# Performance work log

Hardware: AMD Instinct MI355X
Metric: run time of the kernel (lower is better)

## Reference

```python
import jax, jax.numpy as jnp
import numpy as np

N_NODES = 100000
N_EDGES = 800000
N_GRAPHS = 256
IN_C = 96
HID = 96
OUT_C = 16


def setup_inputs() -> dict:
    key = jax.random.key(0)
    ks = jax.random.split(key, 10)
    x = jax.random.normal(ks[0], (N_NODES, IN_C), dtype=jnp.float32)
    edge_index = jax.random.randint(ks[1], (2, N_EDGES), 0, N_NODES, dtype=jnp.int64)
    batch = jnp.sort(jax.random.randint(ks[2], (N_NODES,), 0, N_GRAPHS, dtype=jnp.int64))
    def glorot(k, fan_in, fan_out):
        s = np.sqrt(6.0 / (fan_in + fan_out)).astype(np.float32)
        return jax.random.uniform(k, (fan_in, fan_out), minval=-s, maxval=s, dtype=jnp.float32)
    W1 = glorot(ks[3], IN_C, HID)
    W2 = glorot(ks[4], HID, HID)
    W3 = glorot(ks[5], HID, HID)
    Wlin = glorot(ks[6], HID, OUT_C)
    b1 = jnp.zeros((HID,), dtype=jnp.float32)
    b2 = jnp.zeros((HID,), dtype=jnp.float32)
    b3 = jnp.zeros((HID,), dtype=jnp.float32)
    return {"x": x, "edge_index": edge_index, "batch": batch,
            "W1": W1, "b1": b1, "W2": W2, "b2": b2, "W3": W3, "b3": b3, "Wlin": Wlin}


def _gcn_conv(x, W, b, src, dst):
    # PyG GCNConv(normalize=True): add self-loops, deg includes self-loop,
    # norm_ij = deg_i^{-1/2} * deg_j^{-1/2}; linear (no bias) then scatter-add; bias after.
    n = x.shape[0]
    deg = jnp.zeros((n,), dtype=x.dtype).at[dst].add(1.0) + 1.0  # +1 self-loop
    dinv = jax.lax.rsqrt(deg)
    h = x @ W                                   # [N, H]
    coef = dinv[src] * dinv[dst]                # [E]
    msg = h[src] * coef[:, None]                # [E, H] gather
    agg = jax.ops.segment_sum(msg, dst, num_segments=n)  # scatter-add
    agg = agg + h * (dinv * dinv)[:, None]      # self-loop contribution
    return agg + b


def reference(x, edge_index, batch, W1, b1, W2, b2, W3, b3, Wlin):
    src, dst = edge_index[0], edge_index[1]
    h = jax.nn.relu(_gcn_conv(x, W1, b1, src, dst))
    h = jax.nn.relu(_gcn_conv(h, W2, b2, src, dst))
    h = _gcn_conv(h, W3, b3, src, dst)
    # global mean pool over graphs
    sums = jax.ops.segment_sum(h, batch, num_segments=N_GRAPHS)
    counts = jax.ops.segment_sum(jnp.ones((h.shape[0],), dtype=h.dtype), batch, num_segments=N_GRAPHS)
    pooled = sums / jnp.maximum(counts, 1.0)[:, None]
    return pooled @ Wlin
```

## Files before the change

kernel.cpp:

```cpp
#include <hip/hip_runtime.h>

#define NN 100000
#define NE 800000
#define NG 256
#define CH 96
#define OC 16
#define NBLK 391
#define TM 128
#define GBLK 782

typedef __attribute__((ext_vector_type(8))) short bf16x8;
typedef __attribute__((ext_vector_type(4))) float f32x4;

__device__ __forceinline__ unsigned short f2bf(float x) {
    unsigned u = __float_as_uint(x);
    return (unsigned short)((u + 0x7fffu + ((u >> 16) & 1u)) >> 16);
}
__device__ __forceinline__ float bf2f(unsigned short h) {
    return __uint_as_float(((unsigned)h) << 16);
}
__device__ __forceinline__ void split8(const float4 a, const float4 b,
                                       bf16x8& hi, bf16x8& lo) {
    float v[8] = {a.x, a.y, a.z, a.w, b.x, b.y, b.z, b.w};
#pragma unroll
    for (int j = 0; j < 8; j++) {
        unsigned short h = f2bf(v[j]);
        hi[j] = (short)h;
        lo[j] = (short)f2bf(v[j] - bf2f(h));
    }
}
__device__ __forceinline__ void unpack8(uint4 v, float* f) {
    f[0] = __uint_as_float(v.x << 16); f[1] = __uint_as_float(v.x & 0xffff0000u);
    f[2] = __uint_as_float(v.y << 16); f[3] = __uint_as_float(v.y & 0xffff0000u);
    f[4] = __uint_as_float(v.z << 16); f[5] = __uint_as_float(v.z & 0xffff0000u);
    f[6] = __uint_as_float(v.w << 16); f[7] = __uint_as_float(v.w & 0xffff0000u);
}

__global__ __launch_bounds__(256) void k_init(int* __restrict__ cntp,
                                              int* __restrict__ gtot,
                                              const float* __restrict__ W1,
                                              const float* __restrict__ W2,
                                              const float* __restrict__ W3,
                                              const float* __restrict__ b3,
                                              const float* __restrict__ Wlin,
                                              unsigned short* __restrict__ WH,
                                              unsigned short* __restrict__ WL,
                                              float* __restrict__ b3p) {
    int id = blockIdx.x * 256 + threadIdx.x;
    if (id < NN) {
        uint4 z = {0u, 0u, 0u, 0u};
        uint4* p = reinterpret_cast<uint4*>(&cntp[(size_t)id * 16]);
        p[0] = z; p[1] = z; p[2] = z; p[3] = z;
    }
    if (id == 0) *gtot = 0;
    if (id < 2 * CH * CH) {
        int w = id / (CH * CH);
        int r = id - w * (CH * CH);
        int k = r / CH;
        int n = r - k * CH;
        const float* Ws = (w == 0) ? W1 : W2;
        float v = Ws[k * CH + n];
        unsigned short h = f2bf(v);
        WH[w * CH * CH + n * CH + k] = h;
        WL[w * CH * CH + n * CH + k] = f2bf(v - bf2f(h));
    } else if (id < 2 * CH * CH + CH * OC) {
        int r = id - 2 * CH * CH;
        int k = r / OC;
        int oc = r - k * OC;
        float v = 0.0f;
#pragma unroll 8
        for (int m = 0; m < CH; m++) v += W3[k * CH + m] * Wlin[m * OC + oc];
        unsigned short h = f2bf(v);
        WH[2 * CH * CH + oc * CH + k] = h;
        WL[2 * CH * CH + oc * CH + k] = f2bf(v - bf2f(h));
    } else if (id < 2 * CH * CH + CH * OC + OC) {
        int oc = id - 2 * CH * CH - CH * OC;
        float v = 0.0f;
#pragma unroll 8
        for (int m = 0; m < CH; m++) v += b3[m] * Wlin[m * OC + oc];
        b3p[oc] = v;
    }
}

__global__ __launch_bounds__(256) void k_front(const float* __restrict__ X,
                                               const unsigned short* __restrict__ WH,
                                               const unsigned short* __restrict__ WL,
                                               unsigned short* __restrict__ H,
                                               const int* __restrict__ dst,
                                               int* __restrict__ cntp,
                                               int* __restrict__ slot) {
    __shared__ __align__(16) unsigned short WsH[CH * CH];
    __shared__ __align__(16) unsigned short WsL[CH * CH];

    const int tid = threadIdx.x;

    if (blockIdx.x >= GBLK) {
        int e = (blockIdx.x - GBLK) * 256 + tid;
        slot[e] = atomicAdd(&cntp[(size_t)dst[e] * 16], 1);
        return;
    }

    const int n0 = blockIdx.x * TM;
    {
        const uint4* sH = reinterpret_cast<const uint4*>(WH);
        const uint4* sL = reinterpret_cast<const uint4*>(WL);
        uint4* dH = reinterpret_cast<uint4*>(WsH);
        uint4* dL = reinterpret_cast<uint4*>(WsL);
        for (int i = tid; i < CH * CH / 8; i += 256) {
            dH[i] = sH[i];
            dL[i] = sL[i];
        }
    }
    __syncthreads();

    const int lane = tid & 63;
    const int wave = tid >> 6;
    const int lrow = lane & 15;
    const int quad = lane >> 4;

    const float4* X4 = reinterpret_cast<const float4*>(X);

    f32x4 acc[2][6];
#pragma unroll
    for (int rt = 0; rt < 2; rt++)
#pragma unroll
        for (int ct = 0; ct < 6; ct++) acc[rt][ct] = (f32x4){0.f, 0.f, 0.f, 0.f};

    int arow[2];
#pragma unroll
    for (int rt = 0; rt < 2; rt++)
        arow[rt] = min(n0 + (wave * 2 + rt) * 16 + lrow, NN - 1);

#pragma unroll
    for (int kc = 0; kc < 3; kc++) {
        bf16x8 ahi[2], alo[2];
#pragma unroll
        for (int rt = 0; rt < 2; rt++) {
            int fo = (arow[rt] * CH + kc * 32 + quad * 8) >> 2;
            split8(X4[fo], X4[fo + 1], ahi[rt], alo[rt]);
        }
#pragma unroll
        for (int ct = 0; ct < 6; ct++) {
            int bo = (ct * 16 + lrow) * CH + kc * 32 + quad * 8;
            bf16x8 bhi = *reinterpret_cast<const bf16x8*>(&WsH[bo]);
            bf16x8 blo = *reinterpret_cast<const bf16x8*>(&WsL[bo]);
#pragma unroll
            for (int rt = 0; rt < 2; rt++) {
                acc[rt][ct] = __builtin_amdgcn_mfma_f32_16x16x32_bf16(
                    alo[rt], bhi, acc[rt][ct], 0, 0, 0);
                acc[rt][ct] = __builtin_amdgcn_mfma_f32_16x16x32_bf16(
                    ahi[rt], blo, acc[rt][ct], 0, 0, 0);
                acc[rt][ct] = __builtin_amdgcn_mfma_f32_16x16x32_bf16(
                    ahi[rt], bhi, acc[rt][ct], 0, 0, 0);
            }
        }
    }

#pragma unroll
    for (int rt = 0; rt < 2; rt++) {
        int rbase = n0 + (wave * 2 + rt) * 16 + quad * 4;
#pragma unroll
        for (int ct = 0; ct < 6; ct++) {
            int col = ct * 16 + lrow;
#pragma unroll
            for (int r = 0; r < 4; r++) {
                int row = rbase + r;
                if (row < NN) H[(size_t)row * CH + col] = f2bf(acc[rt][ct][r]);
            }
        }
    }
}

__global__ __launch_bounds__(256) void k_offsets(const int* __restrict__ cntp,
                                                 int* __restrict__ cntc,
                                                 int* __restrict__ gtot,
                                                 int* __restrict__ off,
                                                 float* __restrict__ dinv,
                                                 const int* __restrict__ batch,
                                                 int* __restrict__ goff) {
    int i = blockIdx.x * 256 + threadIdx.x;
    int lane = threadIdx.x & 63;
    int c = (i < NN) ? cntp[(size_t)i * 16] : 0;

    int incl = c;
#pragma unroll
    for (int d = 1; d < 64; d <<= 1) {
        int t = __shfl_up(incl, d);
        if (lane >= d) incl += t;
    }
    int total = __shfl(incl, 63);
    int base = 0;
    if (lane == 63) base = atomicAdd(gtot, total);
    base = __shfl(base, 63);

    if (i >= NN) return;
    cntc[i] = c;
    off[i] = base + incl - c;
    dinv[i] = rsqrtf((float)c + 1.0f);
    int b = batch[i];
    int bp = (i > 0) ? batch[i - 1] : -1;
    for (int g = bp + 1; g <= b; g++) goff[g] = i;
    if (i == NN - 1)
        for (int g = b + 1; g <= NG; g++) goff[g] = NN;
}

__global__ __launch_bounds__(256) void k_build(const int* __restrict__ src,
                                               const int* __restrict__ dst,
                                               const int* __restrict__ off,
                                               const int* __restrict__ slot,
                                               const float* __restrict__ dinv,
                                               float2* __restrict__ packed) {
    int e = blockIdx.x * 256 + threadIdx.x;
    int s = src[e];
    int d = dst[e];
    packed[off[d] + slot[e]] = make_float2(__int_as_float(s), dinv[s] * dinv[d]);
}

__global__ __launch_bounds__(256) void k_gemm_bf16(const unsigned short* __restrict__ X,
                                                   const unsigned short* __restrict__ WH,
                                                   const unsigned short* __restrict__ WL,
                                                   unsigned short* __restrict__ H) {
    __shared__ __align__(16) unsigned short WsH[CH * CH];
    __shared__ __align__(16) unsigned short WsL[CH * CH];

    const int tid = threadIdx.x;
    const int n0 = blockIdx.x * TM;

    {
        const uint4* sH = reinterpret_cast<const uint4*>(WH);
        const uint4* sL = reinterpret_cast<const uint4*>(WL);
        uint4* dH = reinterpret_cast<uint4*>(WsH);
        uint4* dL = reinterpret_cast<uint4*>(WsL);
        for (int i = tid; i < CH * CH / 8; i += 256) {
            dH[i] = sH[i];
            dL[i] = sL[i];
        }
    }
    __syncthreads();

    const int lane = tid & 63;
    const int wave = tid >> 6;
    const int lrow = lane & 15;
    const int quad = lane >> 4;

    f32x4 acc[2][6];
#pragma unroll
    for (int rt = 0; rt < 2; rt++)
#pragma unroll
        for (int ct = 0; ct < 6; ct++) acc[rt][ct] = (f32x4){0.f, 0.f, 0.f, 0.f};

    int arow[2];
#pragma unroll
    for (int rt = 0; rt < 2; rt++)
        arow[rt] = min(n0 + (wave * 2 + rt) * 16 + lrow, NN - 1);

#pragma unroll
    for (int kc = 0; kc < 3; kc++) {
        bf16x8 ahi[2];
#pragma unroll
        for (int rt = 0; rt < 2; rt++)
            ahi[rt] = *reinterpret_cast<const bf16x8*>(
                &X[(size_t)arow[rt] * CH + kc * 32 + quad * 8]);
#pragma unroll
        for (int ct = 0; ct < 6; ct++) {
            int bo = (ct * 16 + lrow) * CH + kc * 32 + quad * 8;
            bf16x8 bhi = *reinterpret_cast<const bf16x8*>(&WsH[bo]);
            bf16x8 blo = *reinterpret_cast<const bf16x8*>(&WsL[bo]);
#pragma unroll
            for (int rt = 0; rt < 2; rt++) {
                acc[rt][ct] = __builtin_amdgcn_mfma_f32_16x16x32_bf16(
                    ahi[rt], blo, acc[rt][ct], 0, 0, 0);
                acc[rt][ct] = __builtin_amdgcn_mfma_f32_16x16x32_bf16(
                    ahi[rt], bhi, acc[rt][ct], 0, 0, 0);
            }
        }
    }

#pragma unroll
    for (int rt = 0; rt < 2; rt++) {
        int rbase = n0 + (wave * 2 + rt) * 16 + quad * 4;
#pragma unroll
        for (int ct = 0; ct < 6; ct++) {
            int col = ct * 16 + lrow;
#pragma unroll
            for (int r = 0; r < 4; r++) {
                int row = rbase + r;
                if (row < NN) H[(size_t)row * CH + col] = f2bf(acc[rt][ct][r]);
            }
        }
    }
}

__global__ __launch_bounds__(256) void k_gemm3(const unsigned short* __restrict__ X,
                                               const unsigned short* __restrict__ WH,
                                               const unsigned short* __restrict__ WL,
                                               unsigned short* __restrict__ H3) {
    __shared__ __align__(16) unsigned short WsH[OC * CH];
    __shared__ __align__(16) unsigned short WsL[OC * CH];

    const int tid = threadIdx.x;
    const int n0 = blockIdx.x * TM;

    {
        const uint4* sH = reinterpret_cast<const uint4*>(WH);
        const uint4* sL = reinterpret_cast<const uint4*>(WL);
        uint4* dH = reinterpret_cast<uint4*>(WsH);
        uint4* dL = reinterpret_cast<uint4*>(WsL);
        for (int i = tid; i < OC * CH / 8; i += 256) {
            dH[i] = sH[i];
            dL[i] = sL[i];
        }
    }
    __syncthreads();

    const int lane = tid & 63;
    const int wave = tid >> 6;
    const int lrow = lane & 15;
    const int quad = lane >> 4;

    f32x4 acc[2];
#pragma unroll
    for (int rt = 0; rt < 2; rt++) acc[rt] = (f32x4){0.f, 0.f, 0.f, 0.f};

    int arow[2];
#pragma unroll
    for (int rt = 0; rt < 2; rt++)
        arow[rt] = min(n0 + (wave * 2 + rt) * 16 + lrow, NN - 1);

#pragma unroll
    for (int kc = 0; kc < 3; kc++) {
        bf16x8 ahi[2];
#pragma unroll
        for (int rt = 0; rt < 2; rt++)
            ahi[rt] = *reinterpret_cast<const bf16x8*>(
                &X[(size_t)arow[rt] * CH + kc * 32 + quad * 8]);
        int bo = lrow * CH + kc * 32 + quad * 8;
        bf16x8 bhi = *reinterpret_cast<const bf16x8*>(&WsH[bo]);
        bf16x8 blo = *reinterpret_cast<const bf16x8*>(&WsL[bo]);
#pragma unroll
        for (int rt = 0; rt < 2; rt++) {
            acc[rt] = __builtin_amdgcn_mfma_f32_16x16x32_bf16(ahi[rt], blo, acc[rt], 0, 0, 0);
            acc[rt] = __builtin_amdgcn_mfma_f32_16x16x32_bf16(ahi[rt], bhi, acc[rt], 0, 0, 0);
        }
    }

#pragma unroll
    for (int rt = 0; rt < 2; rt++) {
        int rbase = n0 + (wave * 2 + rt) * 16 + quad * 4;
#pragma unroll
        for (int r = 0; r < 4; r++) {
            int row = rbase + r;
            if (row < NN) H3[(size_t)row * OC + lrow] = f2bf(acc[rt][r]);
        }
    }
}

template <bool RELU>
__global__ __launch_bounds__(256) void k_aggregate(const int* __restrict__ off,
                                                   const int* __restrict__ cnt,
                                                   const float2* __restrict__ packed,
                                                   const float* __restrict__ dinv,
                                                   const float* __restrict__ bias,
                                                   const unsigned short* __restrict__ H,
                                                   unsigned short* __restrict__ Bout) {
    int idx = blockIdx.x * 256 + threadIdx.x;
    if (idx >= NN * 24) return;
    int t2 = idx >> 1;
    int h = idx & 1;
    int n = t2 / 12;
    int c8 = t2 - n * 12;
    int e0 = off[n];
    int c = cnt[n];
    int half = (c + 1) >> 1;
    int es = e0 + (h ? half : 0);
    int ee = h ? (e0 + c) : (e0 + half);

    const uint4* H8 = reinterpret_cast<const uint4*>(H);

    float a[8] = {0.f, 0.f, 0.f, 0.f, 0.f, 0.f, 0.f, 0.f};
    if (h == 0) {
        float hf[8];
        unpack8(H8[(size_t)n * 12 + c8], hf);
        float di = dinv[n];
        float d2 = di * di;
        const float4* bias4 = reinterpret_cast<const float4*>(bias);
        float4 b0 = bias4[c8 * 2], b1 = bias4[c8 * 2 + 1];
        float bf[8] = {b0.x, b0.y, b0.z, b0.w, b1.x, b1.y, b1.z, b1.w};
#pragma unroll
        for (int j = 0; j < 8; j++) a[j] = hf[j] * d2 + bf[j];
    }

    int last = ee - 1;
    for (int e = es; e < ee; e += 4) {
        int i1 = min(e + 1, last);
        int i2 = min(e + 2, last);
        int i3 = min(e + 3, last);
        float2 p0 = packed[e];
        float2 p1 = packed[i1];
        float2 p2 = packed[i2];
        float2 p3 = packed[i3];
        float c1 = (e + 1 <= last) ? p1.y : 0.0f;
        float c2 = (e + 2 <= last) ? p2.y : 0.0f;
        float c3 = (e + 3 <= last) ? p3.y : 0.0f;
        uint4 v0 = H8[(size_t)__float_as_int(p0.x) * 12 + c8];
        uint4 v1 = H8[(size_t)__float_as_int(p1.x) * 12 + c8];
        uint4 v2 = H8[(size_t)__float_as_int(p2.x) * 12 + c8];
        uint4 v3 = H8[(size_t)__float_as_int(p3.x) * 12 + c8];
        float f0[8], f1[8], f2[8], f3[8];
        unpack8(v0, f0); unpack8(v1, f1); unpack8(v2, f2); unpack8(v3, f3);
#pragma unroll
        for (int j = 0; j < 8; j++)
            a[j] += f0[j] * p0.y + f1[j] * c1 + f2[j] * c2 + f3[j] * c3;
    }

#pragma unroll
    for (int j = 0; j < 8; j++) a[j] += __shfl_xor(a[j], 1);

    if (h == 0) {
        if (RELU) {
#pragma unroll
            for (int j = 0; j < 8; j++) a[j] = fmaxf(a[j], 0.0f);
        }
        uint4 o;
        o.x = (unsigned)f2bf(a[0]) | ((unsigned)f2bf(a[1]) << 16);
        o.y = (unsigned)f2bf(a[2]) | ((unsigned)f2bf(a[3]) << 16);
        o.z = (unsigned)f2bf(a[4]) | ((unsigned)f2bf(a[5]) << 16);
        o.w = (unsigned)f2bf(a[6]) | ((unsigned)f2bf(a[7]) << 16);
        reinterpret_cast<uint4*>(Bout)[(size_t)n * 12 + c8] = o;
    }
}

__global__ __launch_bounds__(256) void k_agg16(const int* __restrict__ off,
                                               const int* __restrict__ cnt,
                                               const float2* __restrict__ packed,
                                               const float* __restrict__ dinv,
                                               const unsigned short* __restrict__ H3,
                                               float* __restrict__ B3) {
    int idx = blockIdx.x * 256 + threadIdx.x;
    if (idx >= NN * 4) return;
    int n = idx >> 2;
    int rem = idx & 3;
    int c8 = rem >> 1;
    int h = rem & 1;
    int e0 = off[n];
    int c = cnt[n];
    int half = (c + 1) >> 1;
    int es = e0 + (h ? half : 0);
    int ee = h ? (e0 + c) : (e0 + half);

    const uint4* H8 = reinterpret_cast<const uint4*>(H3);

    float a[8] = {0.f, 0.f, 0.f, 0.f, 0.f, 0.f, 0.f, 0.f};
    if (h == 0) {
        float hf[8];
        unpack8(H8[(size_t)n * 2 + c8], hf);
        float di = dinv[n];
        float d2 = di * di;
#pragma unroll
        for (int j = 0; j < 8; j++) a[j] = hf[j] * d2;
    }

    int last = ee - 1;
    for (int e = es; e < ee; e += 4) {
        int i1 = min(e + 1, last);
        int i2 = min(e + 2, last);
        int i3 = min(e + 3, last);
        float2 p0 = packed[e];
        float2 p1 = packed[i1];
        float2 p2 = packed[i2];
        float2 p3 = packed[i3];
        float c1 = (e + 1 <= last) ? p1.y : 0.0f;
        float c2 = (e + 2 <= last) ? p2.y : 0.0f;
        float c3 = (e + 3 <= last) ? p3.y : 0.0f;
        uint4 v0 = H8[(size_t)__float_as_int(p0.x) * 2 + c8];
        uint4 v1 = H8[(size_t)__float_as_int(p1.x) * 2 + c8];
        uint4 v2 = H8[(size_t)__float_as_int(p2.x) * 2 + c8];
        uint4 v3 = H8[(size_t)__float_as_int(p3.x) * 2 + c8];
        float f0[8], f1[8], f2[8], f3[8];
        unpack8(v0, f0); unpack8(v1, f1); unpack8(v2, f2); unpack8(v3, f3);
#pragma unroll
        for (int j = 0; j < 8; j++)
            a[j] += f0[j] * p0.y + f1[j] * c1 + f2[j] * c2 + f3[j] * c3;
    }

#pragma unroll
    for (int j = 0; j < 8; j++) a[j] += __shfl_xor(a[j], 1);

    if (h == 0) {
        float4* B4 = reinterpret_cast<float4*>(B3);
        B4[(size_t)n * 4 + c8 * 2 + 0] = make_float4(a[0], a[1], a[2], a[3]);
        B4[(size_t)n * 4 + c8 * 2 + 1] = make_float4(a[4], a[5], a[6], a[7]);
    }
}

__global__ __launch_bounds__(256) void k_pool16(const int* __restrict__ goff,
                                                const float* __restrict__ B3,
                                                const float* __restrict__ b3p,
                                                float* __restrict__ out) {
    __shared__ float sh[16][16];
    int g = blockIdx.x;
    int t = threadIdx.x;
    int ch = t & 15;
    int nl = t >> 4;
    int s = goff[g];
    int e = goff[g + 1];

    float acc = 0.0f;
    for (int n = s + nl; n < e; n += 16) acc += B3[(size_t)n * OC + ch];
    sh[nl][ch] = acc;
    __syncthreads();

    if (t < OC) {
        float r = 0.0f;
#pragma unroll
        for (int j = 0; j < 16; j++) r += sh[j][t];
        out[g * OC + t] = r / fmaxf((float)(e - s), 1.0f) + b3p[t];
    }
}

extern "C" void kernel_launch(void* const* d_in, const int* in_sizes, int n_in,
                              void* d_out, int out_size, void* d_ws, size_t ws_size,
                              hipStream_t stream) {
    const float* x = (const float*)d_in[0];
    const int* ei = (const int*)d_in[1];
    const int* src = ei;
    const int* dst = ei + NE;
    const int* batch = (const int*)d_in[2];
    const float* W1 = (const float*)d_in[3];
    const float* b1 = (const float*)d_in[4];
    const float* W2 = (const float*)d_in[5];
    const float* b2 = (const float*)d_in[6];
    const float* W3 = (const float*)d_in[7];
    const float* b3 = (const float*)d_in[8];
    const float* Wlin = (const float*)d_in[9];
    float* out = (float*)d_out;

    char* ws = (char*)d_ws;
    unsigned short* Ha = (unsigned short*)ws;  ws += (size_t)NN * CH * 2;
    unsigned short* Hb = (unsigned short*)ws;  ws += (size_t)NN * CH * 2;
    unsigned short* Bb = (unsigned short*)ws;  ws += (size_t)NN * CH * 2;
    float2* packed = (float2*)ws;   ws += (size_t)NE * 8;
    unsigned short* WH = (unsigned short*)ws;  ws += 3 * CH * CH * 2;
    unsigned short* WL = (unsigned short*)ws;  ws += 3 * CH * CH * 2;
    float* dinv = (float*)ws;       ws += NN * 4;
    int* off = (int*)ws;            ws += NN * 4;
    int* goff = (int*)ws;           ws += 272 * 4;
    int* cntc = (int*)ws;           ws += (NN + 4) * 4;
    int* gtot = cntc + NN;
    float* b3p = (float*)ws;        ws += 64;
    int* cntp = (int*)Hb;
    int* slot = (int*)Bb;
    unsigned short* H3 = Ha;
    float* B3 = (float*)Hb;

    k_init<<<NBLK, 256, 0, stream>>>(cntp, gtot, W1, W2, W3, b3, Wlin, WH, WL, b3p);
    k_front<<<GBLK + NE / 256, 256, 0, stream>>>(x, WH, WL, Ha, dst, cntp, slot);
    k_offsets<<<NBLK, 256, 0, stream>>>(cntp, cntc, gtot, off, dinv, batch, goff);
    k_build<<<NE / 256, 256, 0, stream>>>(src, dst, off, slot, dinv, packed);

    const int ablk = (NN * 24 + 255) / 256;

    k_aggregate<true><<<ablk, 256, 0, stream>>>(off, cntc, packed, dinv, b1, Ha, Bb);
    k_gemm_bf16<<<GBLK, 256, 0, stream>>>(Bb, WH + CH * CH, WL + CH * CH, Hb);
    k_aggregate<true><<<ablk, 256, 0, stream>>>(off, cntc, packed, dinv, b2, Hb, Bb);
    k_gemm3<<<GBLK, 256, 0, stream>>>(Bb, WH + 2 * CH * CH, WL + 2 * CH * CH, H3);
    k_agg16<<<(NN * 4 + 255) / 256, 256, 0, stream>>>(off, cntc, packed, dinv, H3, B3);
    k_pool16<<<NG, 256, 0, stream>>>(goff, B3, b3p, out);
}
```

Baseline: 268.9 us.

## Fold symmetric normalization into GEMM outputs and store only source indices in CSR

Factors the edge coefficient dinv[s]*dinv[d] so that each GEMM pre-scales its output rows by dinv, and each aggregation sums raw neighbor rows and then scales once by dinv[n] before adding bias. The packed edge array then holds only int source indices instead of (src, coef) float2 pairs, which halves that stream. The CSR build is now fused into the first GEMM launch and the histogram runs as its own kernel first, since the first GEMM needs dinv. The risk is a small numerical shift from scaling before the bf16 rounding, and the histogram no longer overlaps with the first GEMM.

```diff
diff --git a/kernel.cpp b/kernel.cpp
--- a/kernel.cpp
+++ b/kernel.cpp
@@ -82,93 +82,11 @@
     }
 }
 
-__global__ __launch_bounds__(256) void k_front(const float* __restrict__ X,
-                                               const unsigned short* __restrict__ WH,
-                                               const unsigned short* __restrict__ WL,
-                                               unsigned short* __restrict__ H,
-                                               const int* __restrict__ dst,
-                                               int* __restrict__ cntp,
-                                               int* __restrict__ slot) {
-    __shared__ __align__(16) unsigned short WsH[CH * CH];
-    __shared__ __align__(16) unsigned short WsL[CH * CH];
-
-    const int tid = threadIdx.x;
-
-    if (blockIdx.x >= GBLK) {
-        int e = (blockIdx.x - GBLK) * 256 + tid;
-        slot[e] = atomicAdd(&cntp[(size_t)dst[e] * 16], 1);
-        return;
-    }
-
-    const int n0 = blockIdx.x * TM;
-    {
-        const uint4* sH = reinterpret_cast<const uint4*>(WH);
-        const uint4* sL = reinterpret_cast<const uint4*>(WL);
-        uint4* dH = reinterpret_cast<uint4*>(WsH);
-        uint4* dL = reinterpret_cast<uint4*>(WsL);
-        for (int i = tid; i < CH * CH / 8; i += 256) {
-            dH[i] = sH[i];
-            dL[i] = sL[i];
-        }
-    }
-    __syncthreads();
-
-    const int lane = tid & 63;
-    const int wave = tid >> 6;
-    const int lrow = lane & 15;
-    const int quad = lane >> 4;
-
-    const float4* X4 = reinterpret_cast<const float4*>(X);
-
-    f32x4 acc[2][6];
-#pragma unroll
-    for (int rt = 0; rt < 2; rt++)
-#pragma unroll
-        for (int ct = 0; ct < 6; ct++) acc[rt][ct] = (f32x4){0.f, 0.f, 0.f, 0.f};
-
-    int arow[2];
-#pragma unroll
-    for (int rt = 0; rt < 2; rt++)
-        arow[rt] = min(n0 + (wave * 2 + rt) * 16 + lrow, NN - 1);
-
-#pragma unroll
-    for (int kc = 0; kc < 3; kc++) {
-        bf16x8 ahi[2], alo[2];
-#pragma unroll
-        for (int rt = 0; rt < 2; rt++) {
-            int fo = (arow[rt] * CH + kc * 32 + quad * 8) >> 2;
-            split8(X4[fo], X4[fo + 1], ahi[rt], alo[rt]);
-        }
-#pragma unroll
-        for (int ct = 0; ct < 6; ct++) {
-            int bo = (ct * 16 + lrow) * CH + kc * 32 + quad * 8;
-            bf16x8 bhi = *reinterpret_cast<const bf16x8*>(&WsH[bo]);
-            bf16x8 blo = *reinterpret_cast<const bf16x8*>(&WsL[bo]);
-#pragma unroll
-            for (int rt = 0; rt < 2; rt++) {
-                acc[rt][ct] = __builtin_amdgcn_mfma_f32_16x16x32_bf16(
-                    alo[rt], bhi, acc[rt][ct], 0, 0, 0);
-                acc[rt][ct] = __builtin_amdgcn_mfma_f32_16x16x32_bf16(
-                    ahi[rt], blo, acc[rt][ct], 0, 0, 0);
-                acc[rt][ct] = __builtin_amdgcn_mfma_f32_16x16x32_bf16(
-                    ahi[rt], bhi, acc[rt][ct], 0, 0, 0);
-            }
-        }
-    }
-
-#pragma unroll
-    for (int rt = 0; rt < 2; rt++) {
-        int rbase = n0 + (wave * 2 + rt) * 16 + quad * 4;
-#pragma unroll
-        for (int ct = 0; ct < 6; ct++) {
-            int col = ct * 16 + lrow;
-#pragma unroll
-            for (int r = 0; r < 4; r++) {
-                int row = rbase + r;
-                if (row < NN) H[(size_t)row * CH + col] = f2bf(acc[rt][ct][r]);
-            }
-        }
-    }
+__global__ __launch_bounds__(256) void k_hist(const int* __restrict__ dst,
+                                              int* __restrict__ cntp,
+                                              int* __restrict__ slot) {
+    int e = blockIdx.x * 256 + threadIdx.x;
+    slot[e] = atomicAdd(&cntp[(size_t)dst[e] * 16], 1);
 }
 
 __global__ __launch_bounds__(256) void k_offsets(const int* __restrict__ cntp,
@@ -204,28 +122,29 @@
         for (int g = b + 1; g <= NG; g++) goff[g] = NN;
 }
 
-__global__ __launch_bounds__(256) void k_build(const int* __restrict__ src,
-                                               const int* __restrict__ dst,
-                                               const int* __restrict__ off,
-                                               const int* __restrict__ slot,
-                                               const float* __restrict__ dinv,
-                                               float2* __restrict__ packed) {
-    int e = blockIdx.x * 256 + threadIdx.x;
-    int s = src[e];
-    int d = dst[e];
-    packed[off[d] + slot[e]] = make_float2(__int_as_float(s), dinv[s] * dinv[d]);
-}
-
-__global__ __launch_bounds__(256) void k_gemm_bf16(const unsigned short* __restrict__ X,
-                                                   const unsigned short* __restrict__ WH,
-                                                   const unsigned short* __restrict__ WL,
-                                                   unsigned short* __restrict__ H) {
+__global__ __launch_bounds__(256) void k_front2(const float* __restrict__ X,
+                                                const unsigned short* __restrict__ WH,
+                                                const unsigned short* __restrict__ WL,
+                                                const float* __restrict__ dinv,
+                                                unsigned short* __restrict__ H,
+                                                const int* __restrict__ src,
+                                                const int* __restrict__ dst,
+                                                const int* __restrict__ off,
+                                                const int* __restrict__ slot,
+                                                int* __restrict__ packed) {
     __shared__ __align__(16) unsigned short WsH[CH * CH];
     __shared__ __align__(16) unsigned short WsL[CH * CH];
 
     const int tid = threadIdx.x;
+
+    if (blockIdx.x >= GBLK) {
+        int e = (blockIdx.x - GBLK) * 256 + tid;
+        int d = dst[e];
+        packed[off[d] + slot[e]] = src[e];
+        return;
+    }
+
     const int n0 = blockIdx.x * TM;
-
     {
         const uint4* sH = reinterpret_cast<const uint4*>(WH);
         const uint4* sL = reinterpret_cast<const uint4*>(WL);
@@ -243,6 +162,94 @@
     const int lrow = lane & 15;
     const int quad = lane >> 4;
 
+    const float4* X4 = reinterpret_cast<const float4*>(X);
+
+    f32x4 acc[2][6];
+#pragma unroll
+    for (int rt = 0; rt < 2; rt++)
+#pragma unroll
+        for (int ct = 0; ct < 6; ct++) acc[rt][ct] = (f32x4){0.f, 0.f, 0.f, 0.f};
+
+    int arow[2];
+    float dsc[2];
+#pragma unroll
+    for (int rt = 0; rt < 2; rt++) {
+        arow[rt] = min(n0 + (wave * 2 + rt) * 16 + lrow, NN - 1);
+        dsc[rt] = dinv[arow[rt]];
+    }
+
+#pragma unroll
+    for (int kc = 0; kc < 3; kc++) {
+        bf16x8 ahi[2], alo[2];
+#pragma unroll
+        for (int rt = 0; rt < 2; rt++) {
+            int fo = (arow[rt] * CH + kc * 32 + quad * 8) >> 2;
+            float4 a0 = X4[fo], b0 = X4[fo + 1];
+            float s = dsc[rt];
+            a0.x *= s; a0.y *= s; a0.z *= s; a0.w *= s;
+            b0.x *= s; b0.y *= s; b0.z *= s; b0.w *= s;
+            split8(a0, b0, ahi[rt], alo[rt]);
+        }
+#pragma unroll
+        for (int ct = 0; ct < 6; ct++) {
+            int bo = (ct * 16 + lrow) * CH + kc * 32 + quad * 8;
+            bf16x8 bhi = *reinterpret_cast<const bf16x8*>(&WsH[bo]);
+            bf16x8 blo = *reinterpret_cast<const bf16x8*>(&WsL[bo]);
+#pragma unroll
+            for (int rt = 0; rt < 2; rt++) {
+                acc[rt][ct] = __builtin_amdgcn_mfma_f32_16x16x32_bf16(
+                    alo[rt], bhi, acc[rt][ct], 0, 0, 0);
+                acc[rt][ct] = __builtin_amdgcn_mfma_f32_16x16x32_bf16(
+                    ahi[rt], blo, acc[rt][ct], 0, 0, 0);
+                acc[rt][ct] = __builtin_amdgcn_mfma_f32_16x16x32_bf16(
+                    ahi[rt], bhi, acc[rt][ct], 0, 0, 0);
+            }
+        }
+    }
+
+#pragma unroll
+    for (int rt = 0; rt < 2; rt++) {
+        int rbase = n0 + (wave * 2 + rt) * 16 + quad * 4;
+#pragma unroll
+        for (int ct = 0; ct < 6; ct++) {
+            int col = ct * 16 + lrow;
+#pragma unroll
+            for (int r = 0; r < 4; r++) {
+                int row = rbase + r;
+                if (row < NN) H[(size_t)row * CH + col] = f2bf(acc[rt][ct][r]);
+            }
+        }
+    }
+}
+
+__global__ __launch_bounds__(256) void k_gemm_bf16(const unsigned short* __restrict__ X,
+                                                   const unsigned short* __restrict__ WH,
+                                                   const unsigned short* __restrict__ WL,
+                                                   const float* __restrict__ dinv,
+                                                   unsigned short* __restrict__ H) {
+    __shared__ __align__(16) unsigned short WsH[CH * CH];
+    __shared__ __align__(16) unsigned short WsL[CH * CH];
+
+    const int tid = threadIdx.x;
+    const int n0 = blockIdx.x * TM;
+
+    {
+        const uint4* sH = reinterpret_cast<const uint4*>(WH);
+        const uint4* sL = reinterpret_cast<const uint4*>(WL);
+        uint4* dH = reinterpret_cast<uint4*>(WsH);
+        uint4* dL = reinterpret_cast<uint4*>(WsL);
+        for (int i = tid; i < CH * CH / 8; i += 256) {
+            dH[i] = sH[i];
+            dL[i] = sL[i];
+        }
+    }
+    __syncthreads();
+
+    const int lane = tid & 63;
+    const int wave = tid >> 6;
+    const int lrow = lane & 15;
+    const int quad = lane >> 4;
+
     f32x4 acc[2][6];
 #pragma unroll
     for (int rt = 0; rt < 2; rt++)
@@ -279,13 +286,17 @@
 #pragma unroll
     for (int rt = 0; rt < 2; rt++) {
         int rbase = n0 + (wave * 2 + rt) * 16 + quad * 4;
+        float dv[4];
+#pragma unroll
+        for (int r = 0; r < 4; r++)
+            dv[r] = (rbase + r < NN) ? dinv[rbase + r] : 0.0f;
 #pragma unroll
         for (int ct = 0; ct < 6; ct++) {
             int col = ct * 16 + lrow;
 #pragma unroll
             for (int r = 0; r < 4; r++) {
                 int row = rbase + r;
-                if (row < NN) H[(size_t)row * CH + col] = f2bf(acc[rt][ct][r]);
+                if (row < NN) H[(size_t)row * CH + col] = f2bf(acc[rt][ct][r] * dv[r]);
             }
         }
     }
@@ -294,6 +305,7 @@
 __global__ __launch_bounds__(256) void k_gemm3(const unsigned short* __restrict__ X,
                                                const unsigned short* __restrict__ WH,
                                                const unsigned short* __restrict__ WL,
+                                               const float* __restrict__ dinv,
                                                unsigned short* __restrict__ H3) {
     __shared__ __align__(16) unsigned short WsH[OC * CH];
     __shared__ __align__(16) unsigned short WsL[OC * CH];
@@ -350,7 +362,7 @@
 #pragma unroll
         for (int r = 0; r < 4; r++) {
             int row = rbase + r;
-            if (row < NN) H3[(size_t)row * OC + lrow] = f2bf(acc[rt][r]);
+            if (row < NN) H3[(size_t)row * OC + lrow] = f2bf(acc[rt][r] * dinv[row]);
         }
     }
 }
@@ -358,7 +370,7 @@
 template <bool RELU>
 __global__ __launch_bounds__(256) void k_aggregate(const int* __restrict__ off,
                                                    const int* __restrict__ cnt,
-                                                   const float2* __restrict__ packed,
+                                                   const int* __restrict__ packed,
                                                    const float* __restrict__ dinv,
                                                    const float* __restrict__ bias,
                                                    const unsigned short* __restrict__ H,
@@ -381,13 +393,8 @@
     if (h == 0) {
         float hf[8];
         unpack8(H8[(size_t)n * 12 + c8], hf);
-        float di = dinv[n];
-        float d2 = di * di;
-        const float4* bias4 = reinterpret_cast<const float4*>(bias);
-        float4 b0 = bias4[c8 * 2], b1 = bias4[c8 * 2 + 1];
-        float bf[8] = {b0.x, b0.y, b0.z, b0.w, b1.x, b1.y, b1.z, b1.w};
-#pragma unroll
-        for (int j = 0; j < 8; j++) a[j] = hf[j] * d2 + bf[j];
+#pragma unroll
+        for (int j = 0; j < 8; j++) a[j] = hf[j];
     }
 
     int last = ee - 1;
@@ -395,28 +402,34 @@
         int i1 = min(e + 1, last);
         int i2 = min(e + 2, last);
         int i3 = min(e + 3, last);
-        float2 p0 = packed[e];
-        float2 p1 = packed[i1];
-        float2 p2 = packed[i2];
-        float2 p3 = packed[i3];
-        float c1 = (e + 1 <= last) ? p1.y : 0.0f;
-        float c2 = (e + 2 <= last) ? p2.y : 0.0f;
-        float c3 = (e + 3 <= last) ? p3.y : 0.0f;
-        uint4 v0 = H8[(size_t)__float_as_int(p0.x) * 12 + c8];
-        uint4 v1 = H8[(size_t)__float_as_int(p1.x) * 12 + c8];
-        uint4 v2 = H8[(size_t)__float_as_int(p2.x) * 12 + c8];
-        uint4 v3 = H8[(size_t)__float_as_int(p3.x) * 12 + c8];
+        int s0 = packed[e];
+        int s1 = packed[i1];
+        int s2 = packed[i2];
+        int s3 = packed[i3];
+        float c1 = (e + 1 <= last) ? 1.0f : 0.0f;
+        float c2 = (e + 2 <= last) ? 1.0f : 0.0f;
+        float c3 = (e + 3 <= last) ? 1.0f : 0.0f;
+        uint4 v0 = H8[(size_t)s0 * 12 + c8];
+        uint4 v1 = H8[(size_t)s1 * 12 + c8];
+        uint4 v2 = H8[(size_t)s2 * 12 + c8];
+        uint4 v3 = H8[(size_t)s3 * 12 + c8];
         float f0[8], f1[8], f2[8], f3[8];
         unpack8(v0, f0); unpack8(v1, f1); unpack8(v2, f2); unpack8(v3, f3);
 #pragma unroll
         for (int j = 0; j < 8; j++)
-            a[j] += f0[j] * p0.y + f1[j] * c1 + f2[j] * c2 + f3[j] * c3;
+            a[j] += f0[j] + f1[j] * c1 + f2[j] * c2 + f3[j] * c3;
     }
 
 #pragma unroll
     for (int j = 0; j < 8; j++) a[j] += __shfl_xor(a[j], 1);
 
     if (h == 0) {
+        float di = dinv[n];
+        const float4* bias4 = reinterpret_cast<const float4*>(bias);
+        float4 b0 = bias4[c8 * 2], b1 = bias4[c8 * 2 + 1];
+        float bf[8] = {b0.x, b0.y, b0.z, b0.w, b1.x, b1.y, b1.z, b1.w};
+#pragma unroll
+        for (int j = 0; j < 8; j++) a[j] = a[j] * di + bf[j];
         if (RELU) {
 #pragma unroll
             for (int j = 0; j < 8; j++) a[j] = fmaxf(a[j], 0.0f);
@@ -432,7 +445,7 @@
 
 __global__ __launch_bounds__(256) void k_agg16(const int* __restrict__ off,
                                                const int* __restrict__ cnt,
-                                               const float2* __restrict__ packed,
+                                               const int* __restrict__ packed,
                                                const float* __restrict__ dinv,
                                                const unsigned short* __restrict__ H3,
                                                float* __restrict__ B3) {
@@ -454,10 +467,8 @@
     if (h == 0) {
         float hf[8];
         unpack8(H8[(size_t)n * 2 + c8], hf);
-        float di = dinv[n];
-        float d2 = di * di;
-#pragma unroll
-        for (int j = 0; j < 8; j++) a[j] = hf[j] * d2;
+#pragma unroll
+        for (int j = 0; j < 8; j++) a[j] = hf[j];
     }
 
     int last = ee - 1;
@@ -465,28 +476,31 @@
         int i1 = min(e + 1, last);
         int i2 = min(e + 2, last);
         int i3 = min(e + 3, last);
-        float2 p0 = packed[e];
-        float2 p1 = packed[i1];
-        float2 p2 = packed[i2];
-        float2 p3 = packed[i3];
-        float c1 = (e + 1 <= last) ? p1.y : 0.0f;
-        float c2 = (e + 2 <= last) ? p2.y : 0.0f;
-        float c3 = (e + 3 <= last) ? p3.y : 0.0f;
-        uint4 v0 = H8[(size_t)__float_as_int(p0.x) * 2 + c8];
-        uint4 v1 = H8[(size_t)__float_as_int(p1.x) * 2 + c8];
-        uint4 v2 = H8[(size_t)__float_as_int(p2.x) * 2 + c8];
-        uint4 v3 = H8[(size_t)__float_as_int(p3.x) * 2 + c8];
+        int s0 = packed[e];
+        int s1 = packed[i1];
+        int s2 = packed[i2];
+        int s3 = packed[i3];
+        float c1 = (e + 1 <= last) ? 1.0f : 0.0f;
+        float c2 = (e + 2 <= last) ? 1.0f : 0.0f;
+        float c3 = (e + 3 <= last) ? 1.0f : 0.0f;
+        uint4 v0 = H8[(size_t)s0 * 2 + c8];
+        uint4 v1 = H8[(size_t)s1 * 2 + c8];
+        uint4 v2 = H8[(size_t)s2 * 2 + c8];
+        uint4 v3 = H8[(size_t)s3 * 2 + c8];
         float f0[8], f1[8], f2[8], f3[8];
         unpack8(v0, f0); unpack8(v1, f1); unpack8(v2, f2); unpack8(v3, f3);
 #pragma unroll
         for (int j = 0; j < 8; j++)
-            a[j] += f0[j] * p0.y + f1[j] * c1 + f2[j] * c2 + f3[j] * c3;
+            a[j] += f0[j] + f1[j] * c1 + f2[j] * c2 + f3[j] * c3;
     }
 
 #pragma unroll
     for (int j = 0; j < 8; j++) a[j] += __shfl_xor(a[j], 1);
 
     if (h == 0) {
+        float di = dinv[n];
+#pragma unroll
+        for (int j = 0; j < 8; j++) a[j] *= di;
         float4* B4 = reinterpret_cast<float4*>(B3);
         B4[(size_t)n * 4 + c8 * 2 + 0] = make_float4(a[0], a[1], a[2], a[3]);
         B4[(size_t)n * 4 + c8 * 2 + 1] = make_float4(a[4], a[5], a[6], a[7]);
@@ -539,7 +553,7 @@
     unsigned short* Ha = (unsigned short*)ws;  ws += (size_t)NN * CH * 2;
     unsigned short* Hb = (unsigned short*)ws;  ws += (size_t)NN * CH * 2;
     unsigned short* Bb = (unsigned short*)ws;  ws += (size_t)NN * CH * 2;
-    float2* packed = (float2*)ws;   ws += (size_t)NE * 8;
+    int* packed = (int*)ws;         ws += (size_t)NE * 4;
     unsigned short* WH = (unsigned short*)ws;  ws += 3 * CH * CH * 2;
     unsigned short* WL = (unsigned short*)ws;  ws += 3 * CH * CH * 2;
     float* dinv = (float*)ws;       ws += NN * 4;
@@ -554,16 +568,17 @@
     float* B3 = (float*)Hb;
 
     k_init<<<NBLK, 256, 0, stream>>>(cntp, gtot, W1, W2, W3, b3, Wlin, WH, WL, b3p);
-    k_front<<<GBLK + NE / 256, 256, 0, stream>>>(x, WH, WL, Ha, dst, cntp, slot);
+    k_hist<<<NE / 256, 256, 0, stream>>>(dst, cntp, slot);
     k_offsets<<<NBLK, 256, 0, stream>>>(cntp, cntc, gtot, off, dinv, batch, goff);
-    k_build<<<NE / 256, 256, 0, stream>>>(src, dst, off, slot, dinv, packed);
+    k_front2<<<GBLK + NE / 256, 256, 0, stream>>>(x, WH, WL, dinv, Ha,
+                                                  src, dst, off, slot, packed);
 
     const int ablk = (NN * 24 + 255) / 256;
 
     k_aggregate<true><<<ablk, 256, 0, stream>>>(off, cntc, packed, dinv, b1, Ha, Bb);
-    k_gemm_bf16<<<GBLK, 256, 0, stream>>>(Bb, WH + CH * CH, WL + CH * CH, Hb);
+    k_gemm_bf16<<<GBLK, 256, 0, stream>>>(Bb, WH + CH * CH, WL + CH * CH, dinv, Hb);
     k_aggregate<true><<<ablk, 256, 0, stream>>>(off, cntc, packed, dinv, b2, Hb, Bb);
-    k_gemm3<<<GBLK, 256, 0, stream>>>(Bb, WH + 2 * CH * CH, WL + 2 * CH * CH, H3);
+    k_gemm3<<<GBLK, 256, 0, stream>>>(Bb, WH + 2 * CH * CH, WL + 2 * CH * CH, dinv, H3);
     k_agg16<<<(NN * 4 + 255) / 256, 256, 0, stream>>>(off, cntc, packed, dinv, H3, B3);
     k_pool16<<<NG, 256, 0, stream>>>(goff, B3, b3p, out);
 }
```

Result: slower. 282.6 us (+5.1%).
